# Kernel optimization log

Hardware: AMD Instinct MI355X
Metric: run time of the kernel (lower is better)

The kernel has to match this reference:

```python
import jax, jax.numpy as jnp
import numpy as np

H, W = 4096, 4096
KH, KW = 15, 15


def setup_inputs() -> dict:
    key = jax.random.key(0)
    k1, k2 = jax.random.split(key)
    x = jax.random.normal(k1, (H, W), dtype=jnp.float32)
    weight = jax.random.normal(k2, (KH, KW), dtype=jnp.float32)
    bias = jnp.zeros((1,), dtype=jnp.float32)
    return {"x": x, "weight": weight, "bias": bias}


def reference(x, weight, bias):
    # corr2d: valid cross-correlation of 2D x with 2D kernel, output [H-KH+1, W-KW+1]
    # lax conv with NCHW/OIHW layout computes cross-correlation (no kernel flip),
    # identical to the torch per-pixel slice-multiply-sum loop.
    out = jax.lax.conv_general_dilated(
        x[None, None, :, :],            # [1,1,H,W]
        weight[None, None, :, :],       # [1,1,KH,KW]
        window_strides=(1, 1),
        padding="VALID",
    )[0, 0]                             # [H-KH+1, W-KW+1]
    return out + bias  # bias is shape [1], broadcasts like torch
```

## Files before the change

kernel.cpp:

```cpp
#include <hip/hip_runtime.h>


#define HIN 4096
#define WIN 4096
#define KH 15
#define KW 15
#define OH (HIN - KH + 1)
#define OW (WIN - KW + 1)

#define BX 128
#define BY 128
#define XROWS (BY + KH - 1)
#define XCOLS 144
#define LDSW 152
#define NSLOT (XROWS * (XCOLS / 4))

typedef short bf16x8 __attribute__((ext_vector_type(8)));
typedef float f32x4  __attribute__((ext_vector_type(4)));

static __device__ inline short f2bf(float f) {
    unsigned u = __float_as_uint(f);
    u += 0x7fffu + ((u >> 16) & 1u);
    return (short)(u >> 16);
}

__global__ __launch_bounds__(256)
void conv2d_mfma_big(const float* __restrict__ x,
                     const float* __restrict__ w,
                     const float* __restrict__ bias,
                     float* __restrict__ out) {
    __shared__ short lds[XROWS * LDSW];

    const int tid  = threadIdx.x;
    const int lane = tid & 63;
    const int wv   = tid >> 6;
    const int m    = lane & 15;
    const int q    = lane >> 4;
    const int ox0  = blockIdx.x * BX;
    const int oy0  = blockIdx.y * BY;

    for (int i = 0; i < (NSLOT + 255) / 256; ++i) {
        const int f = tid + i * 256;
        if (f < NSLOT) {
            const int r  = f / (XCOLS / 4);
            const int c4 = (f - r * (XCOLS / 4)) * 4;
            int gy = oy0 + r;
            if (gy > HIN - 1) gy = HIN - 1;
            const int gx = ox0 + c4;
            float4 v;
            if (gx + 3 <= WIN - 1) {
                v = *reinterpret_cast<const float4*>(&x[(size_t)gy * WIN + gx]);
            } else {
                const float* row = &x[(size_t)gy * WIN];
                const int x0 = (gx + 0 > WIN - 1) ? WIN - 1 : gx + 0;
                const int x1 = (gx + 1 > WIN - 1) ? WIN - 1 : gx + 1;
                const int x2 = (gx + 2 > WIN - 1) ? WIN - 1 : gx + 2;
                const int x3 = (gx + 3 > WIN - 1) ? WIN - 1 : gx + 3;
                v = make_float4(row[x0], row[x1], row[x2], row[x3]);
            }
            short4 s;
            s.x = f2bf(v.x); s.y = f2bf(v.y); s.z = f2bf(v.z); s.w = f2bf(v.w);
            *reinterpret_cast<short4*>(&lds[r * LDSW + c4]) = s;
        }
    }

    bf16x8 B[KH];
#pragma unroll
    for (int kh = 0; kh < KH; ++kh) {
#pragma unroll
        for (int j = 0; j < 8; ++j) {
            const int d = q * 8 + j - m;
            B[kh][j] = (d >= 0 && d < KW) ? f2bf(w[kh * KW + d]) : (short)0;
        }
    }

    __syncthreads();

    f32x4 acc[2][8];
#pragma unroll
    for (int rv = 0; rv < 2; ++rv)
#pragma unroll
        for (int t = 0; t < 8; ++t) acc[rv][t] = (f32x4){0.f, 0.f, 0.f, 0.f};

    const short* abase = &lds[(wv * 32 + m) * LDSW + q * 8];
#pragma unroll
    for (int kh = 0; kh < KH; ++kh) {
#pragma unroll
        for (int rv = 0; rv < 2; ++rv) {
#pragma unroll
            for (int t = 0; t < 8; ++t) {
                const bf16x8 a = *reinterpret_cast<const bf16x8*>(
                    abase + (kh + rv * 16) * LDSW + t * 16);
                acc[rv][t] =
                    __builtin_amdgcn_mfma_f32_16x16x32_bf16(a, B[kh], acc[rv][t], 0, 0, 0);
            }
        }
    }

    const float b0 = bias[0];
#pragma unroll
    for (int rv = 0; rv < 2; ++rv) {
        const int row0 = oy0 + wv * 32 + rv * 16 + q * 4;
#pragma unroll
        for (int t = 0; t < 8; ++t) {
            const int col = ox0 + t * 16 + m;
            if (col < OW) {
#pragma unroll
                for (int r = 0; r < 4; ++r) {
                    const int row = row0 + r;
                    if (row < OH)
                        out[(size_t)row * OW + col] = acc[rv][t][r] + b0;
                }
            }
        }
    }
}

extern "C" void kernel_launch(void* const* d_in, const int* in_sizes, int n_in,
                              void* d_out, int out_size, void* d_ws, size_t ws_size,
                              hipStream_t stream) {
    const float* x    = (const float*)d_in[0];
    const float* w    = (const float*)d_in[1];
    const float* bias = (const float*)d_in[2];
    float* out        = (float*)d_out;

    dim3 grid((OW + BX - 1) / BX, (OH + BY - 1) / BY);
    dim3 block(256);
    conv2d_mfma_big<<<grid, block, 0, stream>>>(x, w, bias, out);
}
```

Before: 161.1 us.

## Restructure conv into strip-marching blocks with double-buffered register prefetch

Replaces the 128x128 output tiles with 32-row bands that march across a 768-column strip in four 192-column steps. Each step prefetches the next input window into registers while MFMAs run on the current LDS buffer, then writes it into the other of two LDS buffers. Blocks grow to 512 threads and each wave holds fewer accumulators, which targets higher occupancy. The cost is more halo re-reading: 14 extra rows per 32-row band instead of per 128-row tile, so global reads of the input rise.

```diff
diff --git a/kernel.cpp b/kernel.cpp
--- a/kernel.cpp
+++ b/kernel.cpp
@@ -8,12 +8,16 @@
 #define OH (HIN - KH + 1)
 #define OW (WIN - KW + 1)
 
-#define BX 128
-#define BY 128
-#define XROWS (BY + KH - 1)
-#define XCOLS 144
-#define LDSW 152
-#define NSLOT (XROWS * (XCOLS / 4))
+#define BAND 32
+#define SROWS (BAND + KH - 1)
+#define STEPC 192
+#define NSTEP 4
+#define STRIPC (STEPC * NSTEP)
+#define SCOLS 208
+#define LDSW 216
+#define BUFSH (SROWS * LDSW)
+#define SLOTS (SROWS * (SCOLS / 4))
+#define NPF 5
 
 typedef short bf16x8 __attribute__((ext_vector_type(8)));
 typedef float f32x4  __attribute__((ext_vector_type(4)));
@@ -24,45 +28,36 @@
     return (short)(u >> 16);
 }
 
-__global__ __launch_bounds__(256)
-void conv2d_mfma_big(const float* __restrict__ x,
-                     const float* __restrict__ w,
-                     const float* __restrict__ bias,
-                     float* __restrict__ out) {
-    __shared__ short lds[XROWS * LDSW];
+static __device__ inline float4 load_clamped(const float* __restrict__ x,
+                                             int gy, int gx) {
+    if (gy > HIN - 1) gy = HIN - 1;
+    if (gx + 3 <= WIN - 1) {
+        return *reinterpret_cast<const float4*>(&x[(size_t)gy * WIN + gx]);
+    }
+    const float* row = &x[(size_t)gy * WIN];
+    const int x0 = (gx + 0 > WIN - 1) ? WIN - 1 : gx + 0;
+    const int x1 = (gx + 1 > WIN - 1) ? WIN - 1 : gx + 1;
+    const int x2 = (gx + 2 > WIN - 1) ? WIN - 1 : gx + 2;
+    const int x3 = (gx + 3 > WIN - 1) ? WIN - 1 : gx + 3;
+    return make_float4(row[x0], row[x1], row[x2], row[x3]);
+}
+
+__global__ __launch_bounds__(512, 4)
+void conv2d_mfma_strip(const float* __restrict__ x,
+                       const float* __restrict__ w,
+                       const float* __restrict__ bias,
+                       float* __restrict__ out) {
+    __shared__ short lds[2 * BUFSH];
 
     const int tid  = threadIdx.x;
     const int lane = tid & 63;
     const int wv   = tid >> 6;
     const int m    = lane & 15;
     const int q    = lane >> 4;
-    const int ox0  = blockIdx.x * BX;
-    const int oy0  = blockIdx.y * BY;
-
-    for (int i = 0; i < (NSLOT + 255) / 256; ++i) {
-        const int f = tid + i * 256;
-        if (f < NSLOT) {
-            const int r  = f / (XCOLS / 4);
-            const int c4 = (f - r * (XCOLS / 4)) * 4;
-            int gy = oy0 + r;
-            if (gy > HIN - 1) gy = HIN - 1;
-            const int gx = ox0 + c4;
-            float4 v;
-            if (gx + 3 <= WIN - 1) {
-                v = *reinterpret_cast<const float4*>(&x[(size_t)gy * WIN + gx]);
-            } else {
-                const float* row = &x[(size_t)gy * WIN];
-                const int x0 = (gx + 0 > WIN - 1) ? WIN - 1 : gx + 0;
-                const int x1 = (gx + 1 > WIN - 1) ? WIN - 1 : gx + 1;
-                const int x2 = (gx + 2 > WIN - 1) ? WIN - 1 : gx + 2;
-                const int x3 = (gx + 3 > WIN - 1) ? WIN - 1 : gx + 3;
-                v = make_float4(row[x0], row[x1], row[x2], row[x3]);
-            }
-            short4 s;
-            s.x = f2bf(v.x); s.y = f2bf(v.y); s.z = f2bf(v.z); s.w = f2bf(v.w);
-            *reinterpret_cast<short4*>(&lds[r * LDSW + c4]) = s;
-        }
-    }
+    const int rb   = wv & 1;
+    const int cp   = wv >> 1;
+    const int row0 = blockIdx.x * BAND;
+    const int cbase = blockIdx.y * STRIPC;
 
     bf16x8 B[KH];
 #pragma unroll
@@ -73,46 +68,87 @@
             B[kh][j] = (d >= 0 && d < KW) ? f2bf(w[kh * KW + d]) : (short)0;
         }
     }
+    const float b0 = bias[0];
 
+#pragma unroll
+    for (int i = 0; i < NPF; ++i) {
+        const int f = tid + i * 512;
+        if (f < SLOTS) {
+            const int r  = f / (SCOLS / 4);
+            const int c4 = (f - r * (SCOLS / 4)) * 4;
+            const float4 v = load_clamped(x, row0 + r, cbase + c4);
+            short4 s;
+            s.x = f2bf(v.x); s.y = f2bf(v.y); s.z = f2bf(v.z); s.w = f2bf(v.w);
+            *reinterpret_cast<short4*>(&lds[r * LDSW + c4]) = s;
+        }
+    }
     __syncthreads();
 
-    f32x4 acc[2][8];
+    for (int s = 0; s < NSTEP; ++s) {
+        const short* cur = &lds[(s & 1) * BUFSH];
+        short*       nxt = &lds[((s + 1) & 1) * BUFSH];
+        const int    c0  = cbase + s * STEPC;
+        const bool   pfn = (s + 1 < NSTEP) && (c0 + STEPC < OW);
+
+        float4 pf[NPF];
+        if (pfn) {
 #pragma unroll
-    for (int rv = 0; rv < 2; ++rv)
-#pragma unroll
-        for (int t = 0; t < 8; ++t) acc[rv][t] = (f32x4){0.f, 0.f, 0.f, 0.f};
-
-    const short* abase = &lds[(wv * 32 + m) * LDSW + q * 8];
-#pragma unroll
-    for (int kh = 0; kh < KH; ++kh) {
-#pragma unroll
-        for (int rv = 0; rv < 2; ++rv) {
-#pragma unroll
-            for (int t = 0; t < 8; ++t) {
-                const bf16x8 a = *reinterpret_cast<const bf16x8*>(
-                    abase + (kh + rv * 16) * LDSW + t * 16);
-                acc[rv][t] =
-                    __builtin_amdgcn_mfma_f32_16x16x32_bf16(a, B[kh], acc[rv][t], 0, 0, 0);
-            }
-        }
-    }
-
-    const float b0 = bias[0];
-#pragma unroll
-    for (int rv = 0; rv < 2; ++rv) {
-        const int row0 = oy0 + wv * 32 + rv * 16 + q * 4;
-#pragma unroll
-        for (int t = 0; t < 8; ++t) {
-            const int col = ox0 + t * 16 + m;
-            if (col < OW) {
-#pragma unroll
-                for (int r = 0; r < 4; ++r) {
-                    const int row = row0 + r;
-                    if (row < OH)
-                        out[(size_t)row * OW + col] = acc[rv][t][r] + b0;
+            for (int i = 0; i < NPF; ++i) {
+                const int f = tid + i * 512;
+                if (f < SLOTS) {
+                    const int r  = f / (SCOLS / 4);
+                    const int c4 = (f - r * (SCOLS / 4)) * 4;
+                    pf[i] = load_clamped(x, row0 + r, c0 + STEPC + c4);
                 }
             }
         }
+
+        if (c0 < OW) {
+            f32x4 acc[3];
+#pragma unroll
+            for (int t = 0; t < 3; ++t) acc[t] = (f32x4){0.f, 0.f, 0.f, 0.f};
+
+            const short* abase = cur + (rb * 16 + m) * LDSW + cp * 48 + q * 8;
+#pragma unroll
+            for (int kh = 0; kh < KH; ++kh) {
+#pragma unroll
+                for (int t = 0; t < 3; ++t) {
+                    const bf16x8 a = *reinterpret_cast<const bf16x8*>(
+                        abase + kh * LDSW + t * 16);
+                    acc[t] = __builtin_amdgcn_mfma_f32_16x16x32_bf16(a, B[kh], acc[t], 0, 0, 0);
+                }
+            }
+
+            const int orow0 = row0 + rb * 16 + q * 4;
+#pragma unroll
+            for (int t = 0; t < 3; ++t) {
+                const int col = c0 + cp * 48 + t * 16 + m;
+                if (col < OW) {
+#pragma unroll
+                    for (int r = 0; r < 4; ++r) {
+                        const int row = orow0 + r;
+                        if (row < OH)
+                            out[(size_t)row * OW + col] = acc[t][r] + b0;
+                    }
+                }
+            }
+        }
+
+        if (pfn) {
+#pragma unroll
+            for (int i = 0; i < NPF; ++i) {
+                const int f = tid + i * 512;
+                if (f < SLOTS) {
+                    const int r  = f / (SCOLS / 4);
+                    const int c4 = (f - r * (SCOLS / 4)) * 4;
+                    short4 sv;
+                    sv.x = f2bf(pf[i].x); sv.y = f2bf(pf[i].y);
+                    sv.z = f2bf(pf[i].z); sv.w = f2bf(pf[i].w);
+                    *reinterpret_cast<short4*>(&nxt[r * LDSW + c4]) = sv;
+                }
+            }
+        }
+        __syncthreads();
     }
 }
 
@@ -124,7 +160,7 @@
     const float* bias = (const float*)d_in[2];
     float* out        = (float*)d_out;
 
-    dim3 grid((OW + BX - 1) / BX, (OH + BY - 1) / BY);
-    dim3 block(256);
-    conv2d_mfma_big<<<grid, block, 0, stream>>>(x, w, bias, out);
+    dim3 grid((OH + BAND - 1) / BAND, (OW + STRIPC - 1) / STRIPC);
+    dim3 block(512);
+    conv2d_mfma_strip<<<grid, block, 0, stream>>>(x, w, bias, out);
 }
```

New measurement: 264.6 us. 64.2% more time.
